# Kernel optimization log

Measured on AMD Instinct MI355X. Metric: run time of the kernel, lower is better.

Reference implementation:

```python
import jax, jax.numpy as jnp
import numpy as np

N_NODES = 100000
N_EDGES = 1600000
NUM_GRAPHS = 128
EPS = 1e-5


def setup_inputs() -> dict:
    key = jax.random.key(0)
    ks = jax.random.split(key, 8)
    x = jax.random.normal(ks[0], (N_NODES, 8), dtype=jnp.float32)
    edge_index = jax.random.randint(ks[1], (2, N_EDGES), 0, N_NODES, dtype=jnp.int64)
    batch = jnp.sort(jax.random.randint(ks[2], (N_NODES,), 0, NUM_GRAPHS, dtype=jnp.int64))
    W1_l = jax.random.normal(ks[3], (128, 8), dtype=jnp.float32) * 0.3
    b1 = jnp.zeros((128,), dtype=jnp.float32)
    W1_r = jax.random.normal(ks[4], (128, 8), dtype=jnp.float32) * 0.3
    g1 = jnp.ones((128,), dtype=jnp.float32)
    beta1 = jnp.zeros((128,), dtype=jnp.float32)
    W2_l = jax.random.normal(ks[5], (128, 128), dtype=jnp.float32) * 0.08
    b2 = jnp.zeros((128,), dtype=jnp.float32)
    W2_r = jax.random.normal(ks[6], (128, 128), dtype=jnp.float32) * 0.08
    g2 = jnp.ones((128,), dtype=jnp.float32)
    beta2 = jnp.zeros((128,), dtype=jnp.float32)
    return dict(x=x, edge_index=edge_index, batch=batch,
                W1_l=W1_l, b1=b1, W1_r=W1_r, g1=g1, beta1=beta1,
                W2_l=W2_l, b2=b2, W2_r=W2_r, g2=g2, beta2=beta2)


def _sage_conv(x, src, dst, W_l, b, W_r):
    # PyG SAGEConv: out = lin_l(mean_j x_j) + lin_r(x_i); lin_r has no bias
    msg = x[src]                                              # [E, F]
    agg = jax.ops.segment_sum(msg, dst, num_segments=N_NODES)
    deg = jax.ops.segment_sum(jnp.ones((src.shape[0],), x.dtype), dst,
                              num_segments=N_NODES)
    agg = agg / jnp.maximum(deg, 1.0)[:, None]                # mean aggregation
    return agg @ W_l.T + b + x @ W_r.T


def _batch_norm(h, gamma, beta):
    # training-mode BN over the node dimension
    mu = jnp.mean(h, axis=0)
    var = jnp.mean(jnp.square(h - mu), axis=0)
    return gamma * (h - mu) * jax.lax.rsqrt(var + EPS) + beta


def reference(x, edge_index, batch, W1_l, b1, W1_r, g1, beta1,
              W2_l, b2, W2_r, g2, beta2):
    src, dst = edge_index[0], edge_index[1]
    x1 = jax.nn.relu(_batch_norm(_sage_conv(x, src, dst, W1_l, b1, W1_r), g1, beta1))
    x2 = jax.nn.relu(_batch_norm(_sage_conv(x1, src, dst, W2_l, b2, W2_r), g2, beta2))
    h = x1 + x2  # dropout is identity in eval mode
    # global mean pool per graph
    s = jax.ops.segment_sum(h, batch, num_segments=NUM_GRAPHS)
    cnt = jax.ops.segment_sum(jnp.ones((h.shape[0],), h.dtype), batch,
                              num_segments=NUM_GRAPHS)
    return s / jnp.maximum(cnt, 1.0)[:, None]                 # [NUM_GRAPHS, 128]
```

## Files before the change

### kernel.cpp

```cpp
#include <hip/hip_runtime.h>
#include <cstdint>
#include <cstddef>

namespace {

constexpr int N_NODES = 100000;
constexpr int N_EDGES = 1600000;
constexpr int NUM_GRAPHS = 128;
constexpr int F = 128;
constexpr float BN_EPS = 1e-5f;

constexpr int W_BUCK = 512;
constexpr int NBUCK = (N_NODES + W_BUCK - 1) / W_BUCK;
constexpr int CB = 400;
constexpr int CHUNK = N_EDGES / CB;

constexpr int SL1 = 16;
constexpr int SL2 = 8;
constexpr int STATS_FLOATS = (SL1 + SL2) * 256;

typedef float f32x4 __attribute__((ext_vector_type(4)));
typedef float f32x2 __attribute__((ext_vector_type(2)));
typedef short s16x8 __attribute__((ext_vector_type(8)));
typedef unsigned char uchar;
union B8 { uint4 u; s16x8 s; };

__device__ inline ushort f2bf(float x) {
    uint u = __float_as_uint(x);
    u += 0x7fffu + ((u >> 16) & 1u);
    return (ushort)(u >> 16);
}
__device__ inline float bf2f(ushort s) { return __uint_as_float(((uint)s) << 16); }
__device__ inline uint pack2(float lo, float hi) {
    return (uint)f2bf(lo) | ((uint)f2bf(hi) << 16);
}
__device__ inline float bflo(uint u) { return __uint_as_float(u << 16); }
__device__ inline float bfhi(uint u) { return __uint_as_float(u & 0xffff0000u); }

__device__ inline void acc4f8(float* a, uint u) {
    f32x2 lo = __builtin_amdgcn_cvt_pk_f32_fp8((int)u, false);
    f32x2 hi = __builtin_amdgcn_cvt_pk_f32_fp8((int)u, true);
    a[0] += lo[0]; a[1] += lo[1]; a[2] += hi[0]; a[3] += hi[1];
}
__device__ inline void acc8bf(float* a, uint4 v) {
    a[0] += bflo(v.x); a[1] += bfhi(v.x);
    a[2] += bflo(v.y); a[3] += bfhi(v.y);
    a[4] += bflo(v.z); a[5] += bfhi(v.z);
    a[6] += bflo(v.w); a[7] += bfhi(v.w);
}


constexpr int PB_HIST  = CB;
constexpr int PB_BOUND = (N_NODES + 255) / 256;
constexpr int PB_PB    = 64;
constexpr int PB_PB1   = 16;
constexpr int PB_PX    = (N_NODES + 255) / 256;
constexpr int PB_Z     = (STATS_FLOATS + NUM_GRAPHS * F) / 256;
constexpr int PB_TOTAL = PB_HIST + PB_BOUND + PB_PB + PB_PB1 + PB_PX + PB_Z;

__global__ void __launch_bounds__(256) k_pre(
        const int* __restrict__ ei, int* __restrict__ gcount,
        const int* __restrict__ batch, int* __restrict__ gstart,
        const float* __restrict__ W2l, const float* __restrict__ W2r,
        ushort* __restrict__ Wcat,
        const float* __restrict__ W1l, const float* __restrict__ W1r,
        ushort* __restrict__ Wcat1,
        const float* __restrict__ x, ushort* __restrict__ xbf,
        float* __restrict__ stats, float* __restrict__ outacc) {
    __shared__ int bins[NBUCK];
    int bid = blockIdx.x, t = threadIdx.x;
    if (bid < PB_HIST) {
        for (int i = t; i < NBUCK; i += 256) bins[i] = 0;
        __syncthreads();
        int e0 = bid * CHUNK;
        for (int i = t; i < CHUNK; i += 256)
            atomicAdd(&bins[ei[N_EDGES + e0 + i] >> 9], 1);
        __syncthreads();
        for (int i = t; i < NBUCK; i += 256) gcount[i * CB + bid] = bins[i];
        return;
    }
    bid -= PB_HIST;
    if (bid < PB_BOUND) {
        int i = bid * 256 + t;
        if (i >= N_NODES) return;
        int b = batch[i];
        if (i == 0) {
            for (int g = 0; g <= b; ++g) gstart[g] = 0;
        } else {
            int p = batch[i - 1];
            if (p != b) for (int g = p + 1; g <= b; ++g) gstart[g] = i;
        }
        if (i == N_NODES - 1) {
            for (int g = b + 1; g <= NUM_GRAPHS; ++g) gstart[g] = N_NODES;
        }
        return;
    }
    bid -= PB_BOUND;
    if (bid < PB_PB) {
        int i = bid * 256 + t;
        int f = i >> 7, k = i & 127;
        Wcat[f * 256 + k]       = f2bf(W2l[i]);
        Wcat[f * 256 + 128 + k] = f2bf(W2r[i]);
        return;
    }
    bid -= PB_PB;
    if (bid < PB_PB1) {
        int i = bid * 256 + t;
        int f = i >> 5, k = i & 31;
        float v = (k < 8) ? W1r[f * 8 + k] : ((k < 16) ? W1l[f * 8 + (k - 8)] : 0.f);
        Wcat1[i] = f2bf(v);
        return;
    }
    bid -= PB_PB1;
    if (bid < PB_PX) {
        int n = bid * 256 + t;
        if (n >= N_NODES) return;
        const float4* xp = (const float4*)(x + (size_t)n * 8);
        float4 x0 = xp[0], x1 = xp[1];
        uint4 o = {pack2(x0.x, x0.y), pack2(x0.z, x0.w),
                   pack2(x1.x, x1.y), pack2(x1.z, x1.w)};
        *(uint4*)(xbf + (size_t)n * 8) = o;
        return;
    }
    bid -= PB_PX;
    {
        int i = bid * 256 + t;
        if (i < STATS_FLOATS) stats[i] = 0.f;
        else outacc[i - STATS_FLOATS] = 0.f;
    }
}


__global__ void __launch_bounds__(512) k_scanA(int* __restrict__ g,
                                               int* __restrict__ bsum) {
    __shared__ int tmp[512];
    int b = blockIdx.x, t = threadIdx.x;
    int v = (t < CB) ? g[b * CB + t] : 0;
    tmp[t] = v;
    __syncthreads();
    #pragma unroll
    for (int d = 1; d < 512; d <<= 1) {
        int u = (t >= d) ? tmp[t - d] : 0;
        __syncthreads();
        tmp[t] += u;
        __syncthreads();
    }
    if (t < CB) g[b * CB + t] = tmp[t] - v;
    if (t == 511) bsum[b] = tmp[511];
}

__global__ void __launch_bounds__(256) k_part(const int* __restrict__ ei,
                                              const int* __restrict__ gloc,
                                              const int* __restrict__ bsum,
                                              uint* __restrict__ epk) {
    __shared__ int cur[NBUCK];
    __shared__ int pref[256];
    int t = threadIdx.x;
    int v = (t < NBUCK) ? bsum[t] : 0;
    pref[t] = v;
    __syncthreads();
    #pragma unroll
    for (int d = 1; d < 256; d <<= 1) {
        int u = (t >= d) ? pref[t - d] : 0;
        __syncthreads();
        pref[t] += u;
        __syncthreads();
    }
    if (t < NBUCK) cur[t] = gloc[t * CB + blockIdx.x] + (pref[t] - v);
    __syncthreads();
    int e0 = blockIdx.x * CHUNK;
    for (int i = t; i < CHUNK; i += 256) {
        int d = ei[N_EDGES + e0 + i];
        int s = ei[e0 + i];
        int p = atomicAdd(&cur[d >> 9], 1);
        epk[p] = ((uint)s << 9) | (uint)(d & 511);
    }
}

__global__ void __launch_bounds__(512) k_rank(const uint* __restrict__ epk,
                                              const int* __restrict__ bsum,
                                              int* __restrict__ offs,
                                              int* __restrict__ ssrc,
                                              const float* __restrict__ x,
                                              const ushort* __restrict__ xbf,
                                              ushort* __restrict__ xa) {
    __shared__ int dcnt[W_BUCK];
    __shared__ int tmp[W_BUCK];
    __shared__ int cur[W_BUCK];
    __shared__ int pref[256];
    int b = blockIdx.x, t = threadIdx.x;
    if (t < 256) pref[t] = (t < NBUCK) ? bsum[t] : 0;
    __syncthreads();
    #pragma unroll
    for (int d = 1; d < 256; d <<= 1) {
        int u = (t < 256 && t >= d) ? pref[t - d] : 0;
        __syncthreads();
        if (t < 256) pref[t] += u;
        __syncthreads();
    }
    int s0 = pref[b] - bsum[b];
    int s1 = pref[b];
    dcnt[t] = 0;
    __syncthreads();
    for (int i = s0 + t; i < s1; i += 512)
        atomicAdd(&dcnt[epk[i] & 511u], 1);
    __syncthreads();
    int v = dcnt[t];
    tmp[t] = v;
    __syncthreads();
    #pragma unroll
    for (int d = 1; d < 512; d <<= 1) {
        int u = (t >= d) ? tmp[t - d] : 0;
        __syncthreads();
        tmp[t] += u;
        __syncthreads();
    }
    int start = s0 + tmp[t] - v;
    int node = b * W_BUCK + t;
    if (node <= N_NODES) offs[node] = start;
    cur[t] = start;
    __syncthreads();
    for (int i = s0 + t; i < s1; i += 512) {
        uint u = epk[i];
        int p = atomicAdd(&cur[u & 511u], 1);
        ssrc[p] = (int)(u >> 9);
    }

    __syncthreads();
    if (node >= N_NODES) return;
    int gs = start, ge = start + v;
    float a[8];
    #pragma unroll
    for (int i = 0; i < 8; ++i) a[i] = 0.f;
    int j = gs;
    for (; j + 7 < ge; j += 8) {
        int i0 = ssrc[j],   i1 = ssrc[j+1], i2 = ssrc[j+2], i3 = ssrc[j+3];
        int i4 = ssrc[j+4], i5 = ssrc[j+5], i6 = ssrc[j+6], i7 = ssrc[j+7];
        uint4 v0 = *(const uint4*)(xbf + (size_t)i0 * 8);
        uint4 v1 = *(const uint4*)(xbf + (size_t)i1 * 8);
        uint4 v2 = *(const uint4*)(xbf + (size_t)i2 * 8);
        uint4 v3 = *(const uint4*)(xbf + (size_t)i3 * 8);
        uint4 v4 = *(const uint4*)(xbf + (size_t)i4 * 8);
        uint4 v5 = *(const uint4*)(xbf + (size_t)i5 * 8);
        uint4 v6 = *(const uint4*)(xbf + (size_t)i6 * 8);
        uint4 v7 = *(const uint4*)(xbf + (size_t)i7 * 8);
        acc8bf(a, v0); acc8bf(a, v1); acc8bf(a, v2); acc8bf(a, v3);
        acc8bf(a, v4); acc8bf(a, v5); acc8bf(a, v6); acc8bf(a, v7);
    }
    for (; j + 3 < ge; j += 4) {
        int i0 = ssrc[j], i1 = ssrc[j+1], i2 = ssrc[j+2], i3 = ssrc[j+3];
        uint4 v0 = *(const uint4*)(xbf + (size_t)i0 * 8);
        uint4 v1 = *(const uint4*)(xbf + (size_t)i1 * 8);
        uint4 v2 = *(const uint4*)(xbf + (size_t)i2 * 8);
        uint4 v3 = *(const uint4*)(xbf + (size_t)i3 * 8);
        acc8bf(a, v0); acc8bf(a, v1); acc8bf(a, v2); acc8bf(a, v3);
    }
    for (; j < ge; ++j)
        acc8bf(a, *(const uint4*)(xbf + (size_t)ssrc[j] * 8));
    int dg = ge - gs;
    float inv = 1.0f / (float)(dg > 1 ? dg : 1);
    const float4* xp = (const float4*)(x + (size_t)node * 8);
    float4 x0 = xp[0], x1v = xp[1];
    ushort* row = xa + (size_t)node * 32;
    uint4 o0 = {pack2(x0.x, x0.y), pack2(x0.z, x0.w), pack2(x1v.x, x1v.y), pack2(x1v.z, x1v.w)};
    uint4 o1 = {pack2(a[0]*inv, a[1]*inv), pack2(a[2]*inv, a[3]*inv),
                pack2(a[4]*inv, a[5]*inv), pack2(a[6]*inv, a[7]*inv)};
    uint4 z = {0u, 0u, 0u, 0u};
    *(uint4*)(row)      = o0;
    *(uint4*)(row + 8)  = o1;
    *(uint4*)(row + 16) = z;
    *(uint4*)(row + 24) = z;
}


__global__ void __launch_bounds__(256) k_lin1s(
        const ushort* __restrict__ xa, const ushort* __restrict__ Wcat1,
        const float* __restrict__ b1, float* __restrict__ stats1s) {
    __shared__ float sred[256];
    int tid = threadIdx.x;
    int wave = tid >> 6, lane = tid & 63;
    int quad = lane >> 4, l16 = lane & 15;
    int n0 = blockIdx.x * 64;
    sred[tid] = 0.f;
    __syncthreads();

    int node = n0 + wave * 16 + l16;
    int cn = (node < N_NODES) ? node : N_NODES - 1;
    B8 ta;
    ta.u = *(const uint4*)(xa + (size_t)cn * 32 + quad * 8);

    #pragma unroll
    for (int nt = 0; nt < 8; ++nt) {
        int fb = nt * 16 + l16;
        B8 tb;
        tb.u = *(const uint4*)(Wcat1 + fb * 32 + quad * 8);
        f32x4 acc = {0.f, 0.f, 0.f, 0.f};
        acc = __builtin_amdgcn_mfma_f32_16x16x32_bf16(ta.s, tb.s, acc, 0, 0, 0);
        float bb = b1[fb];
        float ls = 0.f, lq = 0.f;
        #pragma unroll
        for (int r = 0; r < 4; ++r) {
            int rn = n0 + wave * 16 + quad * 4 + r;
            if (rn < N_NODES) {
                float v = bf2f(f2bf(acc[r] + bb));
                ls += v; lq += v * v;
            }
        }
        ls += __shfl_xor(ls, 16); ls += __shfl_xor(ls, 32);
        lq += __shfl_xor(lq, 16); lq += __shfl_xor(lq, 32);
        if (quad == 0) {
            atomicAdd(&sred[fb], ls);
            atomicAdd(&sred[128 + fb], lq);
        }
    }
    __syncthreads();
    atomicAdd(&stats1s[(blockIdx.x & (SL1 - 1)) * 256 + tid], sred[tid]);
}

__global__ void __launch_bounds__(256) k_lin1b(
        const ushort* __restrict__ xa, const ushort* __restrict__ Wcat1,
        const float* __restrict__ b1, const float* __restrict__ stats1s,
        const float* __restrict__ gamma, const float* __restrict__ beta,
        ushort* __restrict__ x1bf, uchar* __restrict__ x1f8) {
    __shared__ ushort sOut[64 * 140];
    __shared__ float sSc[128], sSh[128];
    int tid = threadIdx.x;
    int wave = tid >> 6, lane = tid & 63;
    int quad = lane >> 4, l16 = lane & 15;
    int n0 = blockIdx.x * 64;

    if (tid < 128) {
        float s = 0.f, q = 0.f;
        #pragma unroll
        for (int k = 0; k < SL1; ++k) {
            s += stats1s[k * 256 + tid];
            q += stats1s[k * 256 + 128 + tid];
        }
        float mu  = s * (1.0f / N_NODES);
        float var = q * (1.0f / N_NODES) - mu * mu;
        float sc  = gamma[tid] * rsqrtf(var + BN_EPS);
        sSc[tid] = sc;
        sSh[tid] = beta[tid] - mu * sc;
    }
    __syncthreads();

    int node = n0 + wave * 16 + l16;
    int cn = (node < N_NODES) ? node : N_NODES - 1;
    B8 ta;
    ta.u = *(const uint4*)(xa + (size_t)cn * 32 + quad * 8);

    #pragma unroll
    for (int nt = 0; nt < 8; ++nt) {
        int fb = nt * 16 + l16;
        B8 tb;
        tb.u = *(const uint4*)(Wcat1 + fb * 32 + quad * 8);
        f32x4 acc = {0.f, 0.f, 0.f, 0.f};
        acc = __builtin_amdgcn_mfma_f32_16x16x32_bf16(ta.s, tb.s, acc, 0, 0, 0);
        float bb = b1[fb];
        float sc = sSc[fb], sh = sSh[fb];
        #pragma unroll
        for (int r = 0; r < 4; ++r) {
            int row = wave * 16 + quad * 4 + r;
            float v = bf2f(f2bf(acc[r] + bb));
            float y = fmaxf(0.f, v * sc + sh);
            sOut[row * 140 + fb] = f2bf(y);
        }
    }
    __syncthreads();

    #pragma unroll
    for (int p = 0; p < 4; ++p) {
        int row = p * 16 + (tid >> 4);
        int nd = n0 + row;
        if (nd < N_NODES) {
            int c0 = (tid & 15) * 8;
            uint4 v = *(const uint4*)&sOut[row * 140 + c0];
            *(uint4*)(x1bf + (size_t)nd * F + c0) = v;
            float f0 = bflo(v.x), f1 = bfhi(v.x), f2 = bflo(v.y), f3 = bfhi(v.y);
            float f4 = bflo(v.z), f5 = bfhi(v.z), f6 = bflo(v.w), f7 = bfhi(v.w);
            int p0 = __builtin_amdgcn_cvt_pk_fp8_f32(f0, f1, 0, false);
            p0     = __builtin_amdgcn_cvt_pk_fp8_f32(f2, f3, p0, true);
            int p1 = __builtin_amdgcn_cvt_pk_fp8_f32(f4, f5, 0, false);
            p1     = __builtin_amdgcn_cvt_pk_fp8_f32(f6, f7, p1, true);
            uint2 o8 = {(uint)p0, (uint)p1};
            *(uint2*)(x1f8 + (size_t)nd * F + c0) = o8;
        }
    }
}


__global__ void __launch_bounds__(256) k_agg2(
        const uchar* __restrict__ x1f8, const int* __restrict__ offs,
        const int* __restrict__ ssrc, ushort* __restrict__ agg2bf) {
    int t = threadIdx.x;
    int n = blockIdx.x * 32 + (t >> 3);
    int c16 = (t & 7) * 16;
    int s0 = offs[n], s1 = offs[n + 1];
    float acc[16];
    #pragma unroll
    for (int i = 0; i < 16; ++i) acc[i] = 0.f;
    int j = s0;
    for (; j + 7 < s1; j += 8) {
        int i0 = ssrc[j],   i1 = ssrc[j+1], i2 = ssrc[j+2], i3 = ssrc[j+3];
        int i4 = ssrc[j+4], i5 = ssrc[j+5], i6 = ssrc[j+6], i7 = ssrc[j+7];
        uint4 v0 = *(const uint4*)(x1f8 + (size_t)i0 * F + c16);
        uint4 v1 = *(const uint4*)(x1f8 + (size_t)i1 * F + c16);
        uint4 v2 = *(const uint4*)(x1f8 + (size_t)i2 * F + c16);
        uint4 v3 = *(const uint4*)(x1f8 + (size_t)i3 * F + c16);
        uint4 v4 = *(const uint4*)(x1f8 + (size_t)i4 * F + c16);
        uint4 v5 = *(const uint4*)(x1f8 + (size_t)i5 * F + c16);
        uint4 v6 = *(const uint4*)(x1f8 + (size_t)i6 * F + c16);
        uint4 v7 = *(const uint4*)(x1f8 + (size_t)i7 * F + c16);
        acc4f8(acc, v0.x); acc4f8(acc+4, v0.y); acc4f8(acc+8, v0.z); acc4f8(acc+12, v0.w);
        acc4f8(acc, v1.x); acc4f8(acc+4, v1.y); acc4f8(acc+8, v1.z); acc4f8(acc+12, v1.w);
        acc4f8(acc, v2.x); acc4f8(acc+4, v2.y); acc4f8(acc+8, v2.z); acc4f8(acc+12, v2.w);
        acc4f8(acc, v3.x); acc4f8(acc+4, v3.y); acc4f8(acc+8, v3.z); acc4f8(acc+12, v3.w);
        acc4f8(acc, v4.x); acc4f8(acc+4, v4.y); acc4f8(acc+8, v4.z); acc4f8(acc+12, v4.w);
        acc4f8(acc, v5.x); acc4f8(acc+4, v5.y); acc4f8(acc+8, v5.z); acc4f8(acc+12, v5.w);
        acc4f8(acc, v6.x); acc4f8(acc+4, v6.y); acc4f8(acc+8, v6.z); acc4f8(acc+12, v6.w);
        acc4f8(acc, v7.x); acc4f8(acc+4, v7.y); acc4f8(acc+8, v7.z); acc4f8(acc+12, v7.w);
    }
    for (; j + 3 < s1; j += 4) {
        int i0 = ssrc[j], i1 = ssrc[j+1], i2 = ssrc[j+2], i3 = ssrc[j+3];
        uint4 v0 = *(const uint4*)(x1f8 + (size_t)i0 * F + c16);
        uint4 v1 = *(const uint4*)(x1f8 + (size_t)i1 * F + c16);
        uint4 v2 = *(const uint4*)(x1f8 + (size_t)i2 * F + c16);
        uint4 v3 = *(const uint4*)(x1f8 + (size_t)i3 * F + c16);
        acc4f8(acc, v0.x); acc4f8(acc+4, v0.y); acc4f8(acc+8, v0.z); acc4f8(acc+12, v0.w);
        acc4f8(acc, v1.x); acc4f8(acc+4, v1.y); acc4f8(acc+8, v1.z); acc4f8(acc+12, v1.w);
        acc4f8(acc, v2.x); acc4f8(acc+4, v2.y); acc4f8(acc+8, v2.z); acc4f8(acc+12, v2.w);
        acc4f8(acc, v3.x); acc4f8(acc+4, v3.y); acc4f8(acc+8, v3.z); acc4f8(acc+12, v3.w);
    }
    for (; j < s1; ++j) {
        uint4 v = *(const uint4*)(x1f8 + (size_t)ssrc[j] * F + c16);
        acc4f8(acc, v.x); acc4f8(acc+4, v.y); acc4f8(acc+8, v.z); acc4f8(acc+12, v.w);
    }
    int dg = s1 - s0;
    float inv = 1.0f / (float)(dg > 1 ? dg : 1);
    uint4 o0 = {pack2(acc[0]*inv,  acc[1]*inv),  pack2(acc[2]*inv,  acc[3]*inv),
                pack2(acc[4]*inv,  acc[5]*inv),  pack2(acc[6]*inv,  acc[7]*inv)};
    uint4 o1 = {pack2(acc[8]*inv,  acc[9]*inv),  pack2(acc[10]*inv, acc[11]*inv),
                pack2(acc[12]*inv, acc[13]*inv), pack2(acc[14]*inv, acc[15]*inv)};
    ushort* dst = agg2bf + (size_t)n * F + c16;
    *(uint4*)(dst)     = o0;
    *(uint4*)(dst + 8) = o1;
}

__device__ inline int gSw(int f, int j) { return (f << 5) | ((j + f) & 31); }

__global__ void __launch_bounds__(256, 2) k_lin2(
        const ushort* __restrict__ agg2bf, const ushort* __restrict__ x1bf,
        const ushort* __restrict__ Wcat, const float* __restrict__ b2,
        ushort* __restrict__ h2bf, float* __restrict__ stats2s) {
    __shared__ ushort sB[2048 * 8];
    int tid = threadIdx.x;
    int wave = tid >> 6, lane = tid & 63;
    int quad = lane >> 4, l16 = lane & 15;

    int bid = blockIdx.x;
    int ng, fh;
    if (bid < 768) {
        int g = bid >> 4, i = bid & 15;
        ng = g * 8 + (i & 7);
        fh = i >> 3;
    } else {
        int idx = bid - 768;
        ng = 384 + (idx >> 1);
        fh = idx & 1;
    }
    int fbase = fh * 64;
    int wf = wave & 1, grp = wave >> 1;
    int f0 = wf * 32 + l16;
    int f1 = f0 + 16;

    #pragma unroll
    for (int it = 0; it < 8; ++it) {
        int c = it * 256 + tid;
        int f = c >> 5, j = c & 31;
        uint4 v = *(const uint4*)(Wcat + ((size_t)(fbase + f) * 32 + j) * 8);
        *(uint4*)&sB[gSw(f, j) * 8] = v;
    }
    __syncthreads();

    float bb0 = b2[fbase + f0], bb1 = b2[fbase + f1];
    float s0 = 0.f, s0q = 0.f, s1 = 0.f, s1q = 0.f;
    int n0 = ng * 256 + grp * 128;

    s16x8 aA[8], aB[8];
    auto loadTile = [&](s16x8* a, int nb) {
        int an = nb + l16;
        if (an >= N_NODES) an = N_NODES - 1;
        #pragma unroll
        for (int ks = 0; ks < 8; ++ks) {
            const ushort* src = (ks < 4) ? agg2bf : x1bf;
            B8 tm;
            tm.u = *(const uint4*)(src + (size_t)an * F + (ks & 3) * 32 + quad * 8);
            a[ks] = tm.s;
        }
    };
    auto computeTile = [&](s16x8* a, int nb) {
        f32x4 acc0 = {0,0,0,0}, acc1 = {0,0,0,0};
        #pragma unroll
        for (int ks = 0; ks < 8; ++ks) {
            int j = (ks << 2) + quad;
            B8 tb0, tb1;
            tb0.u = *(const uint4*)&sB[gSw(f0, j) * 8];
            tb1.u = *(const uint4*)&sB[gSw(f1, j) * 8];
            acc0 = __builtin_amdgcn_mfma_f32_16x16x32_bf16(a[ks], tb0.s, acc0, 0, 0, 0);
            acc1 = __builtin_amdgcn_mfma_f32_16x16x32_bf16(a[ks], tb1.s, acc1, 0, 0, 0);
        }
        #pragma unroll
        for (int r = 0; r < 4; ++r) {
            int node = nb + quad * 4 + r;
            if (node < N_NODES) {
                float v0 = acc0[r] + bb0, v1 = acc1[r] + bb1;
                h2bf[(size_t)node * F + fbase + f0] = f2bf(v0);
                h2bf[(size_t)node * F + fbase + f1] = f2bf(v1);
                s0 += v0; s0q += v0 * v0;
                s1 += v1; s1q += v1 * v1;
            }
        }
    };

    loadTile(aA, n0);
    #pragma unroll 1
    for (int p = 0; p < 4; ++p) {
        int nb = n0 + p * 32;
        loadTile(aB, nb + 16);
        computeTile(aA, nb);
        if (p < 3) loadTile(aA, nb + 32);
        computeTile(aB, nb + 16);
    }

    s0  += __shfl_xor(s0, 16);  s0  += __shfl_xor(s0, 32);
    s0q += __shfl_xor(s0q, 16); s0q += __shfl_xor(s0q, 32);
    s1  += __shfl_xor(s1, 16);  s1  += __shfl_xor(s1, 32);
    s1q += __shfl_xor(s1q, 16); s1q += __shfl_xor(s1q, 32);
    if (quad == 0) {
        int slot = (blockIdx.x & (SL2 - 1)) * 256;
        atomicAdd(&stats2s[slot + fbase + f0], s0);
        atomicAdd(&stats2s[slot + 128 + fbase + f0], s0q);
        atomicAdd(&stats2s[slot + fbase + f1], s1);
        atomicAdd(&stats2s[slot + 128 + fbase + f1], s1q);
    }
}


__global__ void k_pool(const ushort* __restrict__ x1bf, const ushort* __restrict__ h2bf,
                       const float* __restrict__ stats2s, const float* __restrict__ gamma2,
                       const float* __restrict__ beta2, const int* __restrict__ batch,
                       float* __restrict__ outacc) {
    int f = threadIdx.x & 127;
    int half = threadIdx.x >> 7;
    float s = 0.f, q = 0.f;
    #pragma unroll
    for (int k = 0; k < SL2; ++k) {
        s += stats2s[k * 256 + f];
        q += stats2s[k * 256 + 128 + f];
    }
    float mu  = s * (1.0f / N_NODES);
    float var = q * (1.0f / N_NODES) - mu * mu;
    float sc  = gamma2[f] * rsqrtf(var + BN_EPS);
    float sh  = beta2[f] - mu * sc;
    int n0 = blockIdx.x * 128 + half * 64;
    if (n0 >= N_NODES) return;
    int n1 = min(n0 + 64, N_NODES);
    float acc = 0.f;
    int curg = batch[n0];
    for (int n = n0; n < n1; ++n) {
        int g = batch[n];
        if (g != curg) {
            atomicAdd(&outacc[curg * F + f], acc);
            acc = 0.f; curg = g;
        }
        float v1 = bf2f(x1bf[(size_t)n * F + f]);
        float v2 = fmaxf(0.f, bf2f(h2bf[(size_t)n * F + f]) * sc + sh);
        acc += v1 + v2;
    }
    atomicAdd(&outacc[curg * F + f], acc);
}

__global__ void k_out(const float* __restrict__ outacc, const int* __restrict__ gstart,
                      float* __restrict__ out) {
    int i = blockIdx.x * 256 + threadIdx.x;
    if (i >= NUM_GRAPHS * F) return;
    int g = i >> 7;
    int c = gstart[g + 1] - gstart[g];
    out[i] = outacc[i] / (float)(c > 1 ? c : 1);
}

}

extern "C" void kernel_launch(void* const* d_in, const int* in_sizes, int n_in,
                              void* d_out, int out_size, void* d_ws, size_t ws_size,
                              hipStream_t stream) {
    const float* x     = (const float*)d_in[0];
    const int*   ei    = (const int*)d_in[1];
    const int*   batch = (const int*)d_in[2];
    const float* W1l   = (const float*)d_in[3];
    const float* b1    = (const float*)d_in[4];
    const float* W1r   = (const float*)d_in[5];
    const float* g1    = (const float*)d_in[6];
    const float* be1   = (const float*)d_in[7];
    const float* W2l   = (const float*)d_in[8];
    const float* b2    = (const float*)d_in[9];
    const float* W2r   = (const float*)d_in[10];
    const float* g2    = (const float*)d_in[11];
    const float* be2   = (const float*)d_in[12];
    float* out = (float*)d_out;

    char* w = (char*)d_ws;
    size_t o = 0;
    auto alloc = [&](size_t bytes) {
        void* p = w + o;
        o += (bytes + 511) & ~(size_t)511;
        return p;
    };
    int*    offs   = (int*)alloc((size_t)(N_NODES + 1) * 4);
    int*    gcount = (int*)alloc((size_t)NBUCK * CB * 4);
    int*    bsum   = (int*)alloc((size_t)NBUCK * 4);
    int*    ssrc   = (int*)alloc((size_t)N_EDGES * 4);
    uint*   epk    = (uint*)alloc((size_t)N_EDGES * 4);
    int*    gstart = (int*)alloc((NUM_GRAPHS + 1) * 4);
    float*  stats  = (float*)alloc((size_t)STATS_FLOATS * 4);
    ushort* Wcat   = (ushort*)alloc((size_t)F * 256 * 2);
    ushort* Wcat1  = (ushort*)alloc((size_t)F * 32 * 2);
    float*  outacc = (float*)alloc((size_t)NUM_GRAPHS * F * 4);
    ushort* xbf    = (ushort*)alloc((size_t)N_NODES * 8 * 2);
    ushort* xa     = (ushort*)alloc((size_t)N_NODES * 32 * 2);
    ushort* x1bf   = (ushort*)alloc((size_t)N_NODES * F * 2);
    uchar*  x1f8   = (uchar*)alloc((size_t)N_NODES * F);
    ushort* agg2bf = (ushort*)alloc((size_t)N_NODES * F * 2);
    ushort* h2bf   = (ushort*)alloc((size_t)N_NODES * F * 2);

    float* stats1s = stats;
    float* stats2s = stats + SL1 * 256;

    k_pre<<<PB_TOTAL, 256, 0, stream>>>(ei, gcount, batch, gstart,
                                        W2l, W2r, Wcat, W1l, W1r, Wcat1,
                                        x, xbf, stats, outacc);

    k_scanA<<<NBUCK, 512, 0, stream>>>(gcount, bsum);
    k_part <<<CB, 256, 0, stream>>>(ei, gcount, bsum, epk);
    k_rank <<<NBUCK, 512, 0, stream>>>(epk, bsum, offs, ssrc, x, xbf, xa);

    k_lin1s<<<(N_NODES + 63) / 64, 256, 0, stream>>>(xa, Wcat1, b1, stats1s);
    k_lin1b<<<(N_NODES + 63) / 64, 256, 0, stream>>>(xa, Wcat1, b1, stats1s,
                                                     g1, be1, x1bf, x1f8);

    k_agg2  <<<N_NODES / 32, 256, 0, stream>>>(x1f8, offs, ssrc, agg2bf);
    k_lin2  <<<((N_NODES + 255) / 256) * 2, 256, 0, stream>>>(agg2bf, x1bf, Wcat, b2,
                                                              h2bf, stats2s);

    k_pool<<<(N_NODES + 127) / 128, 256, 0, stream>>>(x1bf, h2bf, stats2s,
                                                      g2, be2, batch, outacc);
    k_out <<<(NUM_GRAPHS * F + 255) / 256, 256, 0, stream>>>(outacc, gstart, out);
}
```

Measured before the change: 270.7 us.

## Derive layer-1 BatchNorm stats from a 16x16 input Gram matrix

Removes the separate k_lin1s pass that recomputed the layer-1 MFMA product just to gather per-feature sum and sum of squares. k_rank now accumulates the 16-dim input sums and the lower-triangular Gram matrix over all nodes. k_lin1b then recovers mean and variance per output feature as the quadratic form w^T G w plus bias terms. This saves a kernel launch and a full read of xa, but adds 136+16 wave shuffle-reductions per wave in k_rank. The E[x^2]-mu^2 variance formula is more prone to cancellation, and the intermediate bf16 rounding before BN is dropped.

```diff
diff --git a/kernel.cpp b/kernel.cpp
--- a/kernel.cpp
+++ b/kernel.cpp
@@ -15,9 +15,11 @@
 constexpr int CB = 400;
 constexpr int CHUNK = N_EDGES / CB;
 
-constexpr int SL1 = 16;
 constexpr int SL2 = 8;
-constexpr int STATS_FLOATS = (SL1 + SL2) * 256;
+constexpr int GSL = 16;
+constexpr int GST = 152;
+constexpr int GRAM_FLOATS = GSL * GST;
+constexpr int ZTOT = GRAM_FLOATS + SL2 * 256 + NUM_GRAPHS * F;
 
 typedef float f32x4 __attribute__((ext_vector_type(4)));
 typedef float f32x2 __attribute__((ext_vector_type(2)));
@@ -55,7 +57,7 @@
 constexpr int PB_PB    = 64;
 constexpr int PB_PB1   = 16;
 constexpr int PB_PX    = (N_NODES + 255) / 256;
-constexpr int PB_Z     = (STATS_FLOATS + NUM_GRAPHS * F) / 256;
+constexpr int PB_Z     = (ZTOT + 255) / 256;
 constexpr int PB_TOTAL = PB_HIST + PB_BOUND + PB_PB + PB_PB1 + PB_PX + PB_Z;
 
 __global__ void __launch_bounds__(256) k_pre(
@@ -66,7 +68,7 @@
         const float* __restrict__ W1l, const float* __restrict__ W1r,
         ushort* __restrict__ Wcat1,
         const float* __restrict__ x, ushort* __restrict__ xbf,
-        float* __restrict__ stats, float* __restrict__ outacc) {
+        float* __restrict__ zbase) {
     __shared__ int bins[NBUCK];
     int bid = blockIdx.x, t = threadIdx.x;
     if (bid < PB_HIST) {
@@ -125,8 +127,7 @@
     bid -= PB_PX;
     {
         int i = bid * 256 + t;
-        if (i < STATS_FLOATS) stats[i] = 0.f;
-        else outacc[i - STATS_FLOATS] = 0.f;
+        if (i < ZTOT) zbase[i] = 0.f;
     }
 }
 
@@ -183,11 +184,13 @@
                                               int* __restrict__ ssrc,
                                               const float* __restrict__ x,
                                               const ushort* __restrict__ xbf,
-                                              ushort* __restrict__ xa) {
+                                              ushort* __restrict__ xa,
+                                              float* __restrict__ gram1s) {
     __shared__ int dcnt[W_BUCK];
     __shared__ int tmp[W_BUCK];
     __shared__ int cur[W_BUCK];
     __shared__ int pref[256];
+    __shared__ float sG[GST];
     int b = blockIdx.x, t = threadIdx.x;
     if (t < 256) pref[t] = (t < NBUCK) ? bsum[t] : 0;
     __syncthreads();
@@ -201,6 +204,7 @@
     int s0 = pref[b] - bsum[b];
     int s1 = pref[b];
     dcnt[t] = 0;
+    if (t < GST) sG[t] = 0.f;
     __syncthreads();
     for (int i = s0 + t; i < s1; i += 512)
         atomicAdd(&dcnt[epk[i] & 511u], 1);
@@ -227,120 +231,124 @@
     }
 
     __syncthreads();
-    if (node >= N_NODES) return;
-    int gs = start, ge = start + v;
-    float a[8];
-    #pragma unroll
-    for (int i = 0; i < 8; ++i) a[i] = 0.f;
-    int j = gs;
-    for (; j + 7 < ge; j += 8) {
-        int i0 = ssrc[j],   i1 = ssrc[j+1], i2 = ssrc[j+2], i3 = ssrc[j+3];
-        int i4 = ssrc[j+4], i5 = ssrc[j+5], i6 = ssrc[j+6], i7 = ssrc[j+7];
-        uint4 v0 = *(const uint4*)(xbf + (size_t)i0 * 8);
-        uint4 v1 = *(const uint4*)(xbf + (size_t)i1 * 8);
-        uint4 v2 = *(const uint4*)(xbf + (size_t)i2 * 8);
-        uint4 v3 = *(const uint4*)(xbf + (size_t)i3 * 8);
-        uint4 v4 = *(const uint4*)(xbf + (size_t)i4 * 8);
-        uint4 v5 = *(const uint4*)(xbf + (size_t)i5 * 8);
-        uint4 v6 = *(const uint4*)(xbf + (size_t)i6 * 8);
-        uint4 v7 = *(const uint4*)(xbf + (size_t)i7 * 8);
-        acc8bf(a, v0); acc8bf(a, v1); acc8bf(a, v2); acc8bf(a, v3);
-        acc8bf(a, v4); acc8bf(a, v5); acc8bf(a, v6); acc8bf(a, v7);
-    }
-    for (; j + 3 < ge; j += 4) {
-        int i0 = ssrc[j], i1 = ssrc[j+1], i2 = ssrc[j+2], i3 = ssrc[j+3];
-        uint4 v0 = *(const uint4*)(xbf + (size_t)i0 * 8);
-        uint4 v1 = *(const uint4*)(xbf + (size_t)i1 * 8);
-        uint4 v2 = *(const uint4*)(xbf + (size_t)i2 * 8);
-        uint4 v3 = *(const uint4*)(xbf + (size_t)i3 * 8);
-        acc8bf(a, v0); acc8bf(a, v1); acc8bf(a, v2); acc8bf(a, v3);
-    }
-    for (; j < ge; ++j)
-        acc8bf(a, *(const uint4*)(xbf + (size_t)ssrc[j] * 8));
-    int dg = ge - gs;
-    float inv = 1.0f / (float)(dg > 1 ? dg : 1);
-    const float4* xp = (const float4*)(x + (size_t)node * 8);
-    float4 x0 = xp[0], x1v = xp[1];
-    ushort* row = xa + (size_t)node * 32;
-    uint4 o0 = {pack2(x0.x, x0.y), pack2(x0.z, x0.w), pack2(x1v.x, x1v.y), pack2(x1v.z, x1v.w)};
-    uint4 o1 = {pack2(a[0]*inv, a[1]*inv), pack2(a[2]*inv, a[3]*inv),
-                pack2(a[4]*inv, a[5]*inv), pack2(a[6]*inv, a[7]*inv)};
-    uint4 z = {0u, 0u, 0u, 0u};
-    *(uint4*)(row)      = o0;
-    *(uint4*)(row + 8)  = o1;
-    *(uint4*)(row + 16) = z;
-    *(uint4*)(row + 24) = z;
-}
-
-
-__global__ void __launch_bounds__(256) k_lin1s(
-        const ushort* __restrict__ xa, const ushort* __restrict__ Wcat1,
-        const float* __restrict__ b1, float* __restrict__ stats1s) {
-    __shared__ float sred[256];
-    int tid = threadIdx.x;
-    int wave = tid >> 6, lane = tid & 63;
-    int quad = lane >> 4, l16 = lane & 15;
-    int n0 = blockIdx.x * 64;
-    sred[tid] = 0.f;
-    __syncthreads();
-
-    int node = n0 + wave * 16 + l16;
-    int cn = (node < N_NODES) ? node : N_NODES - 1;
-    B8 ta;
-    ta.u = *(const uint4*)(xa + (size_t)cn * 32 + quad * 8);
-
-    #pragma unroll
-    for (int nt = 0; nt < 8; ++nt) {
-        int fb = nt * 16 + l16;
-        B8 tb;
-        tb.u = *(const uint4*)(Wcat1 + fb * 32 + quad * 8);
-        f32x4 acc = {0.f, 0.f, 0.f, 0.f};
-        acc = __builtin_amdgcn_mfma_f32_16x16x32_bf16(ta.s, tb.s, acc, 0, 0, 0);
-        float bb = b1[fb];
-        float ls = 0.f, lq = 0.f;
-        #pragma unroll
-        for (int r = 0; r < 4; ++r) {
-            int rn = n0 + wave * 16 + quad * 4 + r;
-            if (rn < N_NODES) {
-                float v = bf2f(f2bf(acc[r] + bb));
-                ls += v; lq += v * v;
-            }
-        }
-        ls += __shfl_xor(ls, 16); ls += __shfl_xor(ls, 32);
-        lq += __shfl_xor(lq, 16); lq += __shfl_xor(lq, 32);
-        if (quad == 0) {
-            atomicAdd(&sred[fb], ls);
-            atomicAdd(&sred[128 + fb], lq);
-        }
-    }
-    __syncthreads();
-    atomicAdd(&stats1s[(blockIdx.x & (SL1 - 1)) * 256 + tid], sred[tid]);
+    float z[16];
+    #pragma unroll
+    for (int i = 0; i < 16; ++i) z[i] = 0.f;
+    if (node < N_NODES) {
+        int gs = start, ge = start + v;
+        float a[8];
+        #pragma unroll
+        for (int i = 0; i < 8; ++i) a[i] = 0.f;
+        int j = gs;
+        for (; j + 7 < ge; j += 8) {
+            int i0 = ssrc[j],   i1 = ssrc[j+1], i2 = ssrc[j+2], i3 = ssrc[j+3];
+            int i4 = ssrc[j+4], i5 = ssrc[j+5], i6 = ssrc[j+6], i7 = ssrc[j+7];
+            uint4 v0 = *(const uint4*)(xbf + (size_t)i0 * 8);
+            uint4 v1 = *(const uint4*)(xbf + (size_t)i1 * 8);
+            uint4 v2 = *(const uint4*)(xbf + (size_t)i2 * 8);
+            uint4 v3 = *(const uint4*)(xbf + (size_t)i3 * 8);
+            uint4 v4 = *(const uint4*)(xbf + (size_t)i4 * 8);
+            uint4 v5 = *(const uint4*)(xbf + (size_t)i5 * 8);
+            uint4 v6 = *(const uint4*)(xbf + (size_t)i6 * 8);
+            uint4 v7 = *(const uint4*)(xbf + (size_t)i7 * 8);
+            acc8bf(a, v0); acc8bf(a, v1); acc8bf(a, v2); acc8bf(a, v3);
+            acc8bf(a, v4); acc8bf(a, v5); acc8bf(a, v6); acc8bf(a, v7);
+        }
+        for (; j + 3 < ge; j += 4) {
+            int i0 = ssrc[j], i1 = ssrc[j+1], i2 = ssrc[j+2], i3 = ssrc[j+3];
+            uint4 v0 = *(const uint4*)(xbf + (size_t)i0 * 8);
+            uint4 v1 = *(const uint4*)(xbf + (size_t)i1 * 8);
+            uint4 v2 = *(const uint4*)(xbf + (size_t)i2 * 8);
+            uint4 v3 = *(const uint4*)(xbf + (size_t)i3 * 8);
+            acc8bf(a, v0); acc8bf(a, v1); acc8bf(a, v2); acc8bf(a, v3);
+        }
+        for (; j < ge; ++j)
+            acc8bf(a, *(const uint4*)(xbf + (size_t)ssrc[j] * 8));
+        int dg = ge - gs;
+        float inv = 1.0f / (float)(dg > 1 ? dg : 1);
+        const float4* xp = (const float4*)(x + (size_t)node * 8);
+        float4 x0 = xp[0], x1v = xp[1];
+        ushort* row = xa + (size_t)node * 32;
+        uint4 o0 = {pack2(x0.x, x0.y), pack2(x0.z, x0.w),
+                    pack2(x1v.x, x1v.y), pack2(x1v.z, x1v.w)};
+        uint4 o1 = {pack2(a[0]*inv, a[1]*inv), pack2(a[2]*inv, a[3]*inv),
+                    pack2(a[4]*inv, a[5]*inv), pack2(a[6]*inv, a[7]*inv)};
+        uint4 zz = {0u, 0u, 0u, 0u};
+        *(uint4*)(row)      = o0;
+        *(uint4*)(row + 8)  = o1;
+        *(uint4*)(row + 16) = zz;
+        *(uint4*)(row + 24) = zz;
+        z[0] = bflo(o0.x); z[1] = bfhi(o0.x); z[2]  = bflo(o0.y); z[3]  = bfhi(o0.y);
+        z[4] = bflo(o0.z); z[5] = bfhi(o0.z); z[6]  = bflo(o0.w); z[7]  = bfhi(o0.w);
+        z[8] = bflo(o1.x); z[9] = bfhi(o1.x); z[10] = bflo(o1.y); z[11] = bfhi(o1.y);
+        z[12]= bflo(o1.z); z[13]= bfhi(o1.z); z[14] = bflo(o1.w); z[15] = bfhi(o1.w);
+    }
+
+    int lane = t & 63;
+    #pragma unroll
+    for (int i = 0; i < 16; ++i) {
+        #pragma unroll
+        for (int j = 0; j <= i; ++j) {
+            float p = z[i] * z[j];
+            p += __shfl_xor(p, 1);  p += __shfl_xor(p, 2);  p += __shfl_xor(p, 4);
+            p += __shfl_xor(p, 8);  p += __shfl_xor(p, 16); p += __shfl_xor(p, 32);
+            if (lane == 0) atomicAdd(&sG[i * (i + 1) / 2 + j], p);
+        }
+        float s = z[i];
+        s += __shfl_xor(s, 1);  s += __shfl_xor(s, 2);  s += __shfl_xor(s, 4);
+        s += __shfl_xor(s, 8);  s += __shfl_xor(s, 16); s += __shfl_xor(s, 32);
+        if (lane == 0) atomicAdd(&sG[136 + i], s);
+    }
+    __syncthreads();
+    if (t < GST) atomicAdd(&gram1s[(b & (GSL - 1)) * GST + t], sG[t]);
 }
 
 __global__ void __launch_bounds__(256) k_lin1b(
         const ushort* __restrict__ xa, const ushort* __restrict__ Wcat1,
-        const float* __restrict__ b1, const float* __restrict__ stats1s,
+        const float* __restrict__ b1, const float* __restrict__ gram1s,
         const float* __restrict__ gamma, const float* __restrict__ beta,
         ushort* __restrict__ x1bf, uchar* __restrict__ x1f8) {
     __shared__ ushort sOut[64 * 140];
+    __shared__ float gG[GST];
     __shared__ float sSc[128], sSh[128];
     int tid = threadIdx.x;
     int wave = tid >> 6, lane = tid & 63;
     int quad = lane >> 4, l16 = lane & 15;
     int n0 = blockIdx.x * 64;
 
+    if (tid < GST) {
+        float s = 0.f;
+        #pragma unroll
+        for (int k = 0; k < GSL; ++k) s += gram1s[k * GST + tid];
+        gG[tid] = s;
+    }
+    __syncthreads();
     if (tid < 128) {
-        float s = 0.f, q = 0.f;
-        #pragma unroll
-        for (int k = 0; k < SL1; ++k) {
-            s += stats1s[k * 256 + tid];
-            q += stats1s[k * 256 + 128 + tid];
-        }
-        float mu  = s * (1.0f / N_NODES);
-        float var = q * (1.0f / N_NODES) - mu * mu;
-        float sc  = gamma[tid] * rsqrtf(var + BN_EPS);
-        sSc[tid] = sc;
-        sSh[tid] = beta[tid] - mu * sc;
+        int f = tid;
+        float wv[16];
+        #pragma unroll
+        for (int k = 0; k < 16; ++k) wv[k] = bf2f(Wcat1[f * 32 + k]);
+        float dotS = 0.f;
+        #pragma unroll
+        for (int k = 0; k < 16; ++k) dotS += wv[k] * gG[136 + k];
+        float quad2 = 0.f;
+        #pragma unroll
+        for (int i = 0; i < 16; ++i) {
+            float wi = wv[i];
+            quad2 += wi * wi * gG[i * (i + 1) / 2 + i];
+            #pragma unroll
+            for (int j = 0; j < i; ++j)
+                quad2 += 2.f * wi * wv[j] * gG[i * (i + 1) / 2 + j];
+        }
+        float bb = b1[f];
+        float sum   = dotS + (float)N_NODES * bb;
+        float sumsq = quad2 + 2.f * bb * dotS + (float)N_NODES * bb * bb;
+        float mu  = sum * (1.0f / N_NODES);
+        float var = sumsq * (1.0f / N_NODES) - mu * mu;
+        var = fmaxf(var, 0.f);
+        float sc  = gamma[f] * rsqrtf(var + BN_EPS);
+        sSc[f] = sc;
+        sSh[f] = beta[f] - mu * sc;
     }
     __syncthreads();
 
@@ -361,8 +369,7 @@
         #pragma unroll
         for (int r = 0; r < 4; ++r) {
             int row = wave * 16 + quad * 4 + r;
-            float v = bf2f(f2bf(acc[r] + bb));
-            float y = fmaxf(0.f, v * sc + sh);
+            float y = fmaxf(0.f, (acc[r] + bb) * sc + sh);
             sOut[row * 140 + fb] = f2bf(y);
         }
     }
@@ -622,10 +629,11 @@
     int*    ssrc   = (int*)alloc((size_t)N_EDGES * 4);
     uint*   epk    = (uint*)alloc((size_t)N_EDGES * 4);
     int*    gstart = (int*)alloc((NUM_GRAPHS + 1) * 4);
-    float*  stats  = (float*)alloc((size_t)STATS_FLOATS * 4);
+    float*  gram1s  = (float*)alloc((size_t)GRAM_FLOATS * 4);
+    float*  stats2s = (float*)alloc((size_t)SL2 * 256 * 4);
+    float*  outacc  = (float*)alloc((size_t)NUM_GRAPHS * F * 4);
     ushort* Wcat   = (ushort*)alloc((size_t)F * 256 * 2);
     ushort* Wcat1  = (ushort*)alloc((size_t)F * 32 * 2);
-    float*  outacc = (float*)alloc((size_t)NUM_GRAPHS * F * 4);
     ushort* xbf    = (ushort*)alloc((size_t)N_NODES * 8 * 2);
     ushort* xa     = (ushort*)alloc((size_t)N_NODES * 32 * 2);
     ushort* x1bf   = (ushort*)alloc((size_t)N_NODES * F * 2);
@@ -633,19 +641,15 @@
     ushort* agg2bf = (ushort*)alloc((size_t)N_NODES * F * 2);
     ushort* h2bf   = (ushort*)alloc((size_t)N_NODES * F * 2);
 
-    float* stats1s = stats;
-    float* stats2s = stats + SL1 * 256;
-
     k_pre<<<PB_TOTAL, 256, 0, stream>>>(ei, gcount, batch, gstart,
                                         W2l, W2r, Wcat, W1l, W1r, Wcat1,
-                                        x, xbf, stats, outacc);
+                                        x, xbf, gram1s);
 
     k_scanA<<<NBUCK, 512, 0, stream>>>(gcount, bsum);
     k_part <<<CB, 256, 0, stream>>>(ei, gcount, bsum, epk);
-    k_rank <<<NBUCK, 512, 0, stream>>>(epk, bsum, offs, ssrc, x, xbf, xa);
-
-    k_lin1s<<<(N_NODES + 63) / 64, 256, 0, stream>>>(xa, Wcat1, b1, stats1s);
-    k_lin1b<<<(N_NODES + 63) / 64, 256, 0, stream>>>(xa, Wcat1, b1, stats1s,
+    k_rank <<<NBUCK, 512, 0, stream>>>(epk, bsum, offs, ssrc, x, xbf, xa, gram1s);
+
+    k_lin1b<<<(N_NODES + 63) / 64, 256, 0, stream>>>(xa, Wcat1, b1, gram1s,
                                                      g1, be1, x1bf, x1f8);
 
     k_agg2  <<<N_NODES / 32, 256, 0, stream>>>(x1f8, offs, ssrc, agg2bf);
```

New measurement: 292.1 us. 1.08x slower.
